# Kernel optimization log

Hardware: AMD Instinct MI355X
Metric: run time of the kernel (lower is better)

## Reference

```python
import jax, jax.numpy as jnp
import numpy as np

FEAT_STRIDE = 16
ANCHOR_SCALES = (8.0, 16.0, 32.0)
ANCHOR_RATIOS = (0.5, 1.0, 2.0)
PRE_NMS_TOPN = 12000
POST_NMS_TOPN = 2000
NMS_THRESH = 0.7
MIN_SIZE = 16.0


def _mkanchors(ws, hs, cx, cy):
    return np.stack([cx - 0.5 * (ws - 1), cy - 0.5 * (hs - 1),
                     cx + 0.5 * (ws - 1), cy + 0.5 * (hs - 1)], axis=1)


def generate_anchors(base_size=16, ratios=ANCHOR_RATIOS, scales=ANCHOR_SCALES):
    ratios = np.asarray(ratios, np.float32)
    scales = np.asarray(scales, np.float32)
    w = h = float(base_size)
    cx = cy = 0.5 * (base_size - 1)
    size = w * h
    ws = np.round(np.sqrt(size / ratios))
    hs = np.round(ws * ratios)
    ratio_anchors = _mkanchors(ws, hs, cx, cy)
    out = []
    for a in ratio_anchors:
        aw = a[2] - a[0] + 1.0
        ah = a[3] - a[1] + 1.0
        acx = a[0] + 0.5 * (aw - 1)
        acy = a[1] + 0.5 * (ah - 1)
        out.append(_mkanchors(aw * scales, ah * scales, acx, acy))
    return np.concatenate(out, axis=0).astype(np.float32)  # (A, 4)


ANCHORS = generate_anchors(FEAT_STRIDE)
NUM_ANCHORS = ANCHORS.shape[0]  # 9


def _proposal_forward(scores, bbox_deltas, im_info):
    A = NUM_ANCHORS
    fg = scores[:, A:, :, :]                       # (1, A, H, W) foreground scores
    H, W = fg.shape[-2], fg.shape[-1]
    im_h, im_w, im_scale = im_info[0, 0], im_info[0, 1], im_info[0, 2]

    # anchor grid
    sx = jnp.arange(W, dtype=jnp.float32) * FEAT_STRIDE
    sy = jnp.arange(H, dtype=jnp.float32) * FEAT_STRIDE
    gy, gx = jnp.meshgrid(sy, sx, indexing='ij')
    shifts = jnp.stack([gx.ravel(), gy.ravel(), gx.ravel(), gy.ravel()], axis=1)  # (K,4)
    anchors = jnp.asarray(ANCHORS)[None, :, :] + shifts[:, None, :]
    anchors = anchors.reshape(-1, 4)               # (K*A, 4)

    deltas = jnp.transpose(bbox_deltas, (0, 2, 3, 1)).reshape(-1, 4)
    sc = jnp.transpose(fg, (0, 2, 3, 1)).reshape(-1)

    # bbox_transform_inv
    aw = anchors[:, 2] - anchors[:, 0] + 1.0
    ah = anchors[:, 3] - anchors[:, 1] + 1.0
    acx = anchors[:, 0] + 0.5 * aw
    acy = anchors[:, 1] + 0.5 * ah
    pcx = deltas[:, 0] * aw + acx
    pcy = deltas[:, 1] * ah + acy
    pw = jnp.exp(deltas[:, 2]) * aw
    ph = jnp.exp(deltas[:, 3]) * ah
    x1 = pcx - 0.5 * pw
    y1 = pcy - 0.5 * ph
    x2 = pcx + 0.5 * pw
    y2 = pcy + 0.5 * ph

    # clip_boxes (scale slot in the clip call is 1.0 in the original)
    x1 = jnp.clip(x1, 0.0, im_w - 1.0)
    x2 = jnp.clip(x2, 0.0, im_w - 1.0)
    y1 = jnp.clip(y1, 0.0, im_h - 1.0)
    y2 = jnp.clip(y2, 0.0, im_h - 1.0)
    props = jnp.stack([x1, y1, x2, y2], axis=1)

    # _filter_boxes: mask instead of gather (jit-safe fixed shapes)
    ms = MIN_SIZE * im_scale
    valid = ((x2 - x1 + 1.0) >= ms) & ((y2 - y1 + 1.0) >= ms)
    sc_m = jnp.where(valid, sc, -jnp.inf)

    # descending sort + pre-NMS top-k in one shot
    top_sc, order = jax.lax.top_k(sc_m, PRE_NMS_TOPN)
    p = props[order]                               # (preN, 4) sorted by score desc
    vk = valid[order]

    pn = jax.lax.stop_gradient(p)
    areas = (pn[:, 2] - pn[:, 0] + 1.0) * (pn[:, 3] - pn[:, 1] + 1.0)
    xx1 = jnp.maximum(pn[:, 0][:, None], pn[:, 0][None, :])
    yy1 = jnp.maximum(pn[:, 1][:, None], pn[:, 1][None, :])
    xx2 = jnp.minimum(pn[:, 2][:, None], pn[:, 2][None, :])
    yy2 = jnp.minimum(pn[:, 3][:, None], pn[:, 3][None, :])
    inter = jnp.maximum(xx2 - xx1 + 1.0, 0.0) * jnp.maximum(yy2 - yy1 + 1.0, 0.0)
    iou = inter / (areas[:, None] + areas[None, :] - inter)
    sup_mat = iou > NMS_THRESH                     # (preN, preN) bool

    idx = jnp.arange(PRE_NMS_TOPN, dtype=jnp.int32)

    def body(keep, xs):
        sup_row, i = xs
        keep = jnp.where(keep[i], keep & ~(sup_row & (idx > i)), keep)
        return keep, None

    keep, _ = jax.lax.scan(body, vk, (sup_mat, idx))

    # keep[:post_nms_topN] with fixed shapes: rank kept boxes, scatter into slots
    rank = jnp.cumsum(keep.astype(jnp.int32)) - 1
    slot_src = jnp.where(keep & (rank < POST_NMS_TOPN), rank, POST_NMS_TOPN)
    slots = jnp.full((POST_NMS_TOPN,), PRE_NMS_TOPN, jnp.int32).at[slot_src].set(idx, mode='drop')

    p_pad = jnp.concatenate([p, jnp.zeros((1, 4), p.dtype)], axis=0)
    s_pad = jnp.concatenate([top_sc, jnp.zeros((1,), top_sc.dtype)], axis=0)
    boxes = p_pad[slots]
    out_sc = s_pad[slots][:, None]
    rois = jnp.concatenate([jnp.zeros((POST_NMS_TOPN, 1), boxes.dtype), boxes], axis=1)
    return rois, out_sc


def setup_inputs() -> dict:
    key = jax.random.key(0)
    k1, k2 = jax.random.split(key)
    H = W = 512
    scores = jax.random.normal(k1, (1, 2 * NUM_ANCHORS, H, W), jnp.float32)
    bbox_deltas = jax.random.normal(k2, (1, 4 * NUM_ANCHORS, H, W), jnp.float32) * 0.2
    im_info = jnp.array([[float(H * FEAT_STRIDE), float(W * FEAT_STRIDE), 1.0]], jnp.float32)
    return {"scores": scores, "bbox_deltas": bbox_deltas, "im_info": im_info}


def reference(scores, bbox_deltas, im_info):
    return _proposal_forward(scores, bbox_deltas, im_info)
```

## Files before the change

kernel.cpp:

```cpp
#include <hip/hip_runtime.h>
#include <hip/hip_bf16.h>
#include <stdint.h>

#pragma clang fp contract(off)

#define FH 512
#define FW 512
#define NA 9
#define HW (FH*FW)
#define TOTAL (HW*NA)
#define PRE_NMS 12000
#define POST_NMS 2000
#define NMS_WORDS 188
#define MT 12032
#define CAND_MAX 16384
#define NMS_TH 0.7f
#define MIN_SIZE_C 16.0f

__constant__ float ANCH[NA][4] = {
  {-84.f,-40.f,99.f,55.f},
  {-176.f,-88.f,191.f,103.f},
  {-360.f,-184.f,375.f,199.f},
  {-56.f,-56.f,71.f,71.f},
  {-120.f,-120.f,135.f,135.f},
  {-248.f,-248.f,263.f,263.f},
  {-36.f,-80.f,51.f,95.f},
  {-80.f,-168.f,95.f,183.f},
  {-168.f,-344.f,183.f,359.f}
};

__device__ __forceinline__ void decode_box(int a, int h, int w,
    const float* __restrict__ deltas, float im_h, float im_w,
    float& x1, float& y1, float& x2, float& y2) {
  float sx = (float)(w * 16);
  float sy = (float)(h * 16);
  float ax1 = ANCH[a][0] + sx;
  float ay1 = ANCH[a][1] + sy;
  float ax2 = ANCH[a][2] + sx;
  float ay2 = ANCH[a][3] + sy;
  float aw = ax2 - ax1 + 1.0f;
  float ah = ay2 - ay1 + 1.0f;
  float acx = ax1 + 0.5f * aw;
  float acy = ay1 + 0.5f * ah;
  int base = h * FW + w;
  float d0 = deltas[(4*a+0)*HW + base];
  float d1 = deltas[(4*a+1)*HW + base];
  float d2 = deltas[(4*a+2)*HW + base];
  float d3 = deltas[(4*a+3)*HW + base];
  float pcx = d0 * aw + acx;
  float pcy = d1 * ah + acy;
  float pw = expf(d2) * aw;
  float ph = expf(d3) * ah;
  x1 = pcx - 0.5f * pw;
  y1 = pcy - 0.5f * ph;
  x2 = pcx + 0.5f * pw;
  y2 = pcy + 0.5f * ph;
  x1 = fminf(fmaxf(x1, 0.0f), im_w - 1.0f);
  x2 = fminf(fmaxf(x2, 0.0f), im_w - 1.0f);
  y1 = fminf(fmaxf(y1, 0.0f), im_h - 1.0f);
  y2 = fminf(fmaxf(y2, 0.0f), im_h - 1.0f);
}

__global__ void k_keys(const float* __restrict__ scores, const float* __restrict__ deltas,
                       const float* __restrict__ im_info, unsigned* __restrict__ keys,
                       unsigned* __restrict__ hist8) {
  __shared__ unsigned lh[256];
  int t = threadIdx.x;
  lh[t] = 0;
  __syncthreads();
  int base = blockIdx.x * blockDim.x + t;
  float im_h = im_info[0], im_w = im_info[1];
  float ms = MIN_SIZE_C * im_info[2];
  int h = base / FW, w = base % FW;
  for (int a = 0; a < NA; a++) {
    float x1, y1, x2, y2;
    decode_box(a, h, w, deltas, im_h, im_w, x1, y1, x2, y2);
    bool valid = ((x2 - x1 + 1.0f) >= ms) && ((y2 - y1 + 1.0f) >= ms);
    float sc = scores[(NA + a)*HW + base];
    float v = valid ? sc : -INFINITY;
    unsigned u = __float_as_uint(v);
    unsigned mono = (u & 0x80000000u) ? ~u : (u | 0x80000000u);
    keys[base*NA + a] = mono;
    atomicAdd(&lh[mono >> 24], 1u);
  }
  __syncthreads();
  atomicAdd(&hist8[t], lh[t]);
}

__global__ void __launch_bounds__(256) k_refine15(const unsigned* __restrict__ keys,
    const unsigned* __restrict__ hist8, unsigned* __restrict__ hist15) {
  __shared__ unsigned ssum[256];
  __shared__ unsigned sB8;
  int t = threadIdx.x;
  unsigned hv = hist8[t];
  ssum[t] = hv;
  __syncthreads();
  for (int off = 1; off < 256; off <<= 1) {
    unsigned v = ssum[t];
    unsigned add = (t + off < 256) ? ssum[t + off] : 0u;
    __syncthreads();
    ssum[t] = v + add;
    __syncthreads();
  }
  unsigned above = ssum[t] - hv;
  if (above < PRE_NMS && above + hv >= PRE_NMS) sB8 = (unsigned)t;
  __syncthreads();
  unsigned B8 = sB8;
  int stride = gridDim.x * blockDim.x;
  for (int i = blockIdx.x * blockDim.x + t; i < TOTAL; i += stride) {
    unsigned k = keys[i];
    if ((k >> 24) == B8) atomicAdd(&hist15[(k >> 9) & 0x7FFFu], 1u);
  }
}

__global__ void __launch_bounds__(256) k_compact(const unsigned* __restrict__ keys,
    const unsigned* __restrict__ hist8, const unsigned* __restrict__ hist15,
    unsigned* __restrict__ cnt, unsigned long long* __restrict__ cand) {
  __shared__ unsigned ssum[256];
  __shared__ unsigned sB8, sT2, sB15;
  int t = threadIdx.x;
  unsigned hv = hist8[t];
  ssum[t] = hv;
  __syncthreads();
  for (int off = 1; off < 256; off <<= 1) {
    unsigned v = ssum[t];
    unsigned add = (t + off < 256) ? ssum[t + off] : 0u;
    __syncthreads();
    ssum[t] = v + add;
    __syncthreads();
  }
  unsigned above = ssum[t] - hv;
  if (above < PRE_NMS && above + hv >= PRE_NMS) { sB8 = (unsigned)t; sT2 = PRE_NMS - above; }
  __syncthreads();
  unsigned B8 = sB8, T2 = sT2;
  unsigned loc = 0;
  for (int i = 0; i < 128; i++) loc += hist15[t*128 + i];
  __syncthreads();
  ssum[t] = loc;
  __syncthreads();
  for (int off = 1; off < 256; off <<= 1) {
    unsigned v = ssum[t];
    unsigned add = (t + off < 256) ? ssum[t + off] : 0u;
    __syncthreads();
    ssum[t] = v + add;
    __syncthreads();
  }
  unsigned above15 = ssum[t] - loc;
  unsigned acc = above15;
  for (int i = 127; i >= 0; i--) {
    unsigned cb = hist15[t*128 + i];
    acc += cb;
    if (acc >= T2 && acc - cb < T2) sB15 = (unsigned)(t*128 + i);
  }
  __syncthreads();
  unsigned K = (B8 << 24) | (sB15 << 9);
  int stride = gridDim.x * blockDim.x;
  for (int i = blockIdx.x * blockDim.x + t; i < TOTAL; i += stride) {
    unsigned k = keys[i];
    if (k >= K) {
      unsigned pos = atomicAdd(cnt, 1u);
      if (pos < CAND_MAX)
        cand[pos] = ((unsigned long long)k << 32) | (unsigned)(~(unsigned)i);
    }
  }
}

__global__ void __launch_bounds__(256) k_rank(const unsigned* __restrict__ pcnt,
    const unsigned long long* __restrict__ cand,
    const float* __restrict__ deltas, const float* __restrict__ im_info,
    float4* __restrict__ boxes, float* __restrict__ scoresArr,
    unsigned long long* __restrict__ remvInit) {
  __shared__ unsigned long long tile[2048];
  unsigned cnt = *pcnt;
  if (cnt > CAND_MAX) cnt = CAND_MAX;
  int i = blockIdx.x * 256 + threadIdx.x;
  unsigned long long mine = (i < (int)cnt) ? cand[i] : 0ULL;
  int rank = 0;
  for (unsigned t0 = 0; t0 < cnt; t0 += 2048) {
    unsigned n = min(2048u, cnt - t0);
    __syncthreads();
    for (unsigned j = threadIdx.x; j < n; j += 256) tile[j] = cand[t0 + j];
    __syncthreads();
    if (i < (int)cnt) {
      unsigned j = 0;
      #pragma unroll 8
      for (; j < n; j++) rank += (tile[j] > mine) ? 1 : 0;
    }
  }
  if (i < (int)cnt && rank < PRE_NMS) {
    unsigned mono = (unsigned)(mine >> 32);
    unsigned idx = ~(unsigned)(mine & 0xFFFFFFFFull);
    unsigned u = (mono & 0x80000000u) ? (mono ^ 0x80000000u) : ~mono;
    float sc = __uint_as_float(u);
    int a = idx % NA;
    int base = idx / NA;
    int h = base / FW, w = base % FW;
    float x1, y1, x2, y2;
    decode_box(a, h, w, deltas, im_info[0], im_info[1], x1, y1, x2, y2);
    boxes[rank] = make_float4(x1, y1, x2, y2);
    scoresArr[rank] = sc;
    if (!(sc > -INFINITY)) atomicOr(&remvInit[rank >> 6], 1ULL << (rank & 63));
  }
}

__global__ void k_mask(const float4* __restrict__ boxes, unsigned long long* __restrict__ maskT) {
  int bi = blockIdx.y, bj = blockIdx.x;
  if (bj < bi) return;
  __shared__ float4 jb[64];
  int t = threadIdx.x;
  int jg = bj * 64 + t;
  jb[t] = (jg < PRE_NMS) ? boxes[jg] : make_float4(0.f, 0.f, -1.f, -1.f);
  __syncthreads();
  int i = bi * 64 + t;
  if (i >= PRE_NMS) return;
  float4 b = boxes[i];
  float area_i = (b.z - b.x + 1.0f) * (b.w - b.y + 1.0f);
  unsigned long long bits = 0;
  for (int jj = 0; jj < 64; jj++) {
    float4 o = jb[jj];
    float xx1 = fmaxf(b.x, o.x);
    float yy1 = fmaxf(b.y, o.y);
    float xx2 = fminf(b.z, o.z);
    float yy2 = fminf(b.w, o.w);
    float iw = fmaxf(xx2 - xx1 + 1.0f, 0.0f);
    float ih = fmaxf(yy2 - yy1 + 1.0f, 0.0f);
    float inter = iw * ih;
    float area_o = (o.z - o.x + 1.0f) * (o.w - o.y + 1.0f);
    float iou = inter / (area_i + area_o - inter);
    if (iou > NMS_TH) bits |= (1ULL << jj);
  }
  maskT[(size_t)bj * MT + i] = bits;
}

__global__ void __launch_bounds__(64) k_nms(const unsigned long long* __restrict__ maskT,
    const unsigned long long* __restrict__ remvInit,
    const float4* __restrict__ boxes, const float* __restrict__ scoresArr,
    float* __restrict__ out) {
  int lane = threadIdx.x;
  __shared__ unsigned klist[POST_NMS];
  __shared__ unsigned long long gbuf[32 * 128];
  int kept_cnt = 0;
  bool done = false;
  unsigned long long W = remvInit[0];
  unsigned long long diagc = maskT[lane];
  unsigned long long nwc   = maskT[(size_t)MT + lane];
  for (int c = 0; c < NMS_WORDS; c++) {
    bool more = (c + 1 < NMS_WORDS);
    int kc = kept_cnt;
    int nIss = more ? ((kc + 63) >> 6) : 0;
    for (int ii = 0; ii < nIss; ii++) {
      int q = ii * 64 + lane;
      if (q < kc) {
        unsigned j = klist[q];
        const void* g = (const void*)(maskT + (size_t)(c + 1) * MT + (j & ~1u));
        void* l = (void*)((char*)gbuf + ii * 1024);
        __builtin_amdgcn_global_load_lds(
            (const __attribute__((address_space(1))) unsigned*)g,
            (__attribute__((address_space(3))) unsigned*)l, 16, 0, 0);
      }
    }
    unsigned long long diagN = 0, nwN = 0;
    if (more) {
      diagN = maskT[(size_t)(c + 1) * MT + (c + 1) * 64 + lane];
      if (c + 2 < NMS_WORDS) nwN = maskT[(size_t)(c + 2) * MT + (c + 1) * 64 + lane];
    }
    int gi0 = c * 64;
    int jmax = PRE_NMS - gi0; if (jmax > 64) jmax = 64;
    unsigned long long avail = ~W;
    if (jmax < 64) avail &= ((1ULL << jmax) - 1ULL);
    unsigned long long keptmask = 0;
    while (avail) {
      int j = __ffsll((long long)avail) - 1;
      keptmask |= (1ULL << j);
      if (lane == 0) klist[kept_cnt] = (unsigned)(gi0 + j);
      kept_cnt++;
      if (kept_cnt >= POST_NMS) { done = true; break; }
      unsigned long long supp = __shfl(diagc, j);
      avail &= ~supp;
      avail &= ~((2ULL << j) - 1ULL);
    }
    if (done || !more) break;
    unsigned long long x = ((keptmask >> lane) & 1ULL) ? nwc : 0ULL;
    asm volatile("s_waitcnt vmcnt(0)" ::: "memory");
    for (int ii = 0; ii < nIss; ii++) {
      int q = ii * 64 + lane;
      if (q < kc) {
        unsigned j = klist[q];
        x |= gbuf[ii * 128 + lane * 2 + (j & 1u)];
      }
    }
    for (int off = 32; off; off >>= 1) x |= __shfl_xor(x, off);
    W = x | remvInit[c + 1];
    __syncthreads();
    diagc = diagN; nwc = nwN;
  }
  __syncthreads();
  for (int s = lane; s < POST_NMS; s += 64) {
    float x1 = 0.f, y1 = 0.f, x2 = 0.f, y2 = 0.f, sc = 0.f;
    if (s < kept_cnt) {
      unsigned r = klist[s];
      float4 b = boxes[r];
      x1 = b.x; y1 = b.y; x2 = b.z; y2 = b.w;
      sc = scoresArr[r];
    }
    out[s*5 + 0] = 0.f;
    out[s*5 + 1] = x1;
    out[s*5 + 2] = y1;
    out[s*5 + 3] = x2;
    out[s*5 + 4] = y2;
    out[POST_NMS*5 + s] = sc;
  }
}

extern "C" void kernel_launch(void* const* d_in, const int* in_sizes, int n_in,
                              void* d_out, int out_size, void* d_ws, size_t ws_size,
                              hipStream_t stream) {
  const float* scores  = (const float*)d_in[0];
  const float* deltas  = (const float*)d_in[1];
  const float* im_info = (const float*)d_in[2];
  float* out = (float*)d_out;
  char* ws = (char*)d_ws;

  unsigned* keys             = (unsigned*)(ws + 0);
  unsigned* hist8            = (unsigned*)(ws + 9437184);
  unsigned* hist15           = (unsigned*)(ws + 9438208);
  unsigned* scal             = (unsigned*)(ws + 9569280);
  unsigned long long* remvI  = (unsigned long long*)(ws + 9569536);
  unsigned long long* cand   = (unsigned long long*)(ws + 9571072);
  float4* boxes              = (float4*)(ws + 9702144);
  float* scoresArr           = (float*)(ws + 9894144);
  unsigned long long* maskT  = (unsigned long long*)(ws + 9942144);

  hipMemsetAsync(ws + 9437184, 0, 133888, stream);

  k_keys<<<HW/256, 256, 0, stream>>>(scores, deltas, im_info, keys, hist8);
  k_refine15<<<256, 256, 0, stream>>>(keys, hist8, hist15);
  k_compact<<<256, 256, 0, stream>>>(keys, hist8, hist15, &scal[4], cand);
  k_rank<<<CAND_MAX/256, 256, 0, stream>>>(&scal[4], cand, deltas, im_info,
                                           boxes, scoresArr, remvI);
  dim3 mg(NMS_WORDS, NMS_WORDS);
  k_mask<<<mg, 64, 0, stream>>>(boxes, maskT);
  k_nms<<<1, 64, 0, stream>>>(maskT, remvI, boxes, scoresArr, out);
}
```

Measured before the change: 907.2 us.

## Switch NMS mask to row-major layout and accumulate suppression rows in registers

The IoU mask is now stored row-major, with 192 words per box, instead of column-transposed, and k_mask computes 8 column words per workgroup. The single-workgroup NMS loop now stages each newly kept box's full mask row into LDS with global_load_lds. It ORs those rows into per-lane register accumulators, replacing the old per-column gather over every kept box. The remove-init bitmap is now memset to ones and cleared for valid boxes with atomicAnd, and the rank count loop uses four accumulators. The aim is to cut the serial NMS loop's per-iteration work from a cost that grows with the kept count to one row load per newly kept box. The trade-off is more LDS traffic and dynamic shared memory.

```diff
diff --git a/kernel.cpp b/kernel.cpp
--- a/kernel.cpp
+++ b/kernel.cpp
@@ -12,7 +12,7 @@
 #define PRE_NMS 12000
 #define POST_NMS 2000
 #define NMS_WORDS 188
-#define MT 12032
+#define MROW 192
 #define CAND_MAX 16384
 #define NMS_TH 0.7f
 #define MIN_SIZE_C 16.0f
@@ -182,9 +182,17 @@
     for (unsigned j = threadIdx.x; j < n; j += 256) tile[j] = cand[t0 + j];
     __syncthreads();
     if (i < (int)cnt) {
+      int q0 = 0, q1 = 0, q2 = 0, q3 = 0;
       unsigned j = 0;
-      #pragma unroll 8
-      for (; j < n; j++) rank += (tile[j] > mine) ? 1 : 0;
+      #pragma unroll 4
+      for (; j + 4 <= n; j += 4) {
+        q0 += (tile[j]   > mine) ? 1 : 0;
+        q1 += (tile[j+1] > mine) ? 1 : 0;
+        q2 += (tile[j+2] > mine) ? 1 : 0;
+        q3 += (tile[j+3] > mine) ? 1 : 0;
+      }
+      for (; j < n; j++) q0 += (tile[j] > mine) ? 1 : 0;
+      rank += q0 + q1 + q2 + q3;
     }
   }
   if (i < (int)cnt && rank < PRE_NMS) {
@@ -199,70 +207,75 @@
     decode_box(a, h, w, deltas, im_info[0], im_info[1], x1, y1, x2, y2);
     boxes[rank] = make_float4(x1, y1, x2, y2);
     scoresArr[rank] = sc;
-    if (!(sc > -INFINITY)) atomicOr(&remvInit[rank >> 6], 1ULL << (rank & 63));
-  }
-}
-
-__global__ void k_mask(const float4* __restrict__ boxes, unsigned long long* __restrict__ maskT) {
-  int bi = blockIdx.y, bj = blockIdx.x;
-  if (bj < bi) return;
-  __shared__ float4 jb[64];
+    if (sc > -INFINITY)
+      atomicAnd(&remvInit[rank >> 6], ~(1ULL << (rank & 63)));
+  }
+}
+
+__global__ void __launch_bounds__(64) k_mask(const float4* __restrict__ boxes,
+                                             unsigned long long* __restrict__ mask) {
+  int wg = blockIdx.x;
+  int bi = blockIdx.y;
+  if (wg * 8 + 7 < bi) return;
+  __shared__ float4 jb[8][64];
   int t = threadIdx.x;
-  int jg = bj * 64 + t;
-  jb[t] = (jg < PRE_NMS) ? boxes[jg] : make_float4(0.f, 0.f, -1.f, -1.f);
+  #pragma unroll
+  for (int k = 0; k < 8; k++) {
+    int jg = (wg * 8 + k) * 64 + t;
+    jb[k][t] = (jg < PRE_NMS) ? boxes[jg] : make_float4(0.f, 0.f, -1.f, -1.f);
+  }
   __syncthreads();
   int i = bi * 64 + t;
   if (i >= PRE_NMS) return;
   float4 b = boxes[i];
   float area_i = (b.z - b.x + 1.0f) * (b.w - b.y + 1.0f);
-  unsigned long long bits = 0;
-  for (int jj = 0; jj < 64; jj++) {
-    float4 o = jb[jj];
-    float xx1 = fmaxf(b.x, o.x);
-    float yy1 = fmaxf(b.y, o.y);
-    float xx2 = fminf(b.z, o.z);
-    float yy2 = fminf(b.w, o.w);
-    float iw = fmaxf(xx2 - xx1 + 1.0f, 0.0f);
-    float ih = fmaxf(yy2 - yy1 + 1.0f, 0.0f);
-    float inter = iw * ih;
-    float area_o = (o.z - o.x + 1.0f) * (o.w - o.y + 1.0f);
-    float iou = inter / (area_i + area_o - inter);
-    if (iou > NMS_TH) bits |= (1ULL << jj);
-  }
-  maskT[(size_t)bj * MT + i] = bits;
-}
-
-__global__ void __launch_bounds__(64) k_nms(const unsigned long long* __restrict__ maskT,
-    const unsigned long long* __restrict__ remvInit,
+  unsigned long long bits[8];
+  #pragma unroll
+  for (int k = 0; k < 8; k++) {
+    unsigned long long bb = 0;
+    for (int jj = 0; jj < 64; jj++) {
+      float4 o = jb[k][jj];
+      float xx1 = fmaxf(b.x, o.x);
+      float yy1 = fmaxf(b.y, o.y);
+      float xx2 = fminf(b.z, o.z);
+      float yy2 = fminf(b.w, o.w);
+      float iw = fmaxf(xx2 - xx1 + 1.0f, 0.0f);
+      float ih = fmaxf(yy2 - yy1 + 1.0f, 0.0f);
+      float inter = iw * ih;
+      float area_o = (o.z - o.x + 1.0f) * (o.w - o.y + 1.0f);
+      float iou = inter / (area_i + area_o - inter);
+      if (iou > NMS_TH) bb |= (1ULL << jj);
+    }
+    bits[k] = bb;
+  }
+  size_t rb = (size_t)i * MROW + wg * 8;
+  #pragma unroll
+  for (int k = 0; k < 8; k++) mask[rb + k] = bits[k];
+}
+
+__global__ void __launch_bounds__(64) k_nms(const unsigned long long* __restrict__ mask,
+    const unsigned long long* __restrict__ remvI,
     const float4* __restrict__ boxes, const float* __restrict__ scoresArr,
     float* __restrict__ out) {
+  extern __shared__ unsigned long long dyn[];
+  unsigned long long* stage = dyn;
+  unsigned* klist = (unsigned*)(dyn + 64 * MROW);
   int lane = threadIdx.x;
-  __shared__ unsigned klist[POST_NMS];
-  __shared__ unsigned long long gbuf[32 * 128];
-  int kept_cnt = 0;
+  unsigned long long r0 = remvI[lane];
+  unsigned long long r1 = remvI[64 + lane];
+  unsigned long long r2 = remvI[128 + lane];
+  unsigned long long W = __shfl(r0, 0);
+  unsigned long long diagc = mask[(size_t)lane * MROW + 0];
+  unsigned long long nw1c  = mask[(size_t)lane * MROW + 1];
+  int kept_cnt = 0, nkPrev = 0;
   bool done = false;
-  unsigned long long W = remvInit[0];
-  unsigned long long diagc = maskT[lane];
-  unsigned long long nwc   = maskT[(size_t)MT + lane];
   for (int c = 0; c < NMS_WORDS; c++) {
     bool more = (c + 1 < NMS_WORDS);
-    int kc = kept_cnt;
-    int nIss = more ? ((kc + 63) >> 6) : 0;
-    for (int ii = 0; ii < nIss; ii++) {
-      int q = ii * 64 + lane;
-      if (q < kc) {
-        unsigned j = klist[q];
-        const void* g = (const void*)(maskT + (size_t)(c + 1) * MT + (j & ~1u));
-        void* l = (void*)((char*)gbuf + ii * 1024);
-        __builtin_amdgcn_global_load_lds(
-            (const __attribute__((address_space(1))) unsigned*)g,
-            (__attribute__((address_space(3))) unsigned*)l, 16, 0, 0);
-      }
-    }
-    unsigned long long diagN = 0, nwN = 0;
+    unsigned long long diagN = 0, nw1N = 0;
     if (more) {
-      diagN = maskT[(size_t)(c + 1) * MT + (c + 1) * 64 + lane];
-      if (c + 2 < NMS_WORDS) nwN = maskT[(size_t)(c + 2) * MT + (c + 1) * 64 + lane];
+      size_t rb = (size_t)((c + 1) * 64 + lane) * MROW;
+      diagN = mask[rb + (c + 1)];
+      if (c + 2 < NMS_WORDS) nw1N = mask[rb + (c + 2)];
     }
     int gi0 = c * 64;
     int jmax = PRE_NMS - gi0; if (jmax > 64) jmax = 64;
@@ -280,19 +293,37 @@
       avail &= ~((2ULL << j) - 1ULL);
     }
     if (done || !more) break;
-    unsigned long long x = ((keptmask >> lane) & 1ULL) ? nwc : 0ULL;
+    unsigned long long A = ((keptmask >> lane) & 1ULL) ? nw1c : 0ULL;
     asm volatile("s_waitcnt vmcnt(0)" ::: "memory");
-    for (int ii = 0; ii < nIss; ii++) {
-      int q = ii * 64 + lane;
-      if (q < kc) {
-        unsigned j = klist[q];
-        x |= gbuf[ii * 128 + lane * 2 + (j & 1u)];
-      }
-    }
+    __builtin_amdgcn_sched_barrier(0);
+    for (int s = 0; s < nkPrev; s++) {
+      r0 |= stage[s * MROW + lane];
+      r1 |= stage[s * MROW + 64 + lane];
+      r2 |= stage[s * MROW + 128 + lane];
+    }
+    unsigned long long x = A;
+    #pragma unroll
     for (int off = 32; off; off >>= 1) x |= __shfl_xor(x, off);
-    W = x | remvInit[c + 1];
-    __syncthreads();
-    diagc = diagN; nwc = nwN;
+    int cw = c + 1;
+    unsigned long long Rw = ((cw >> 6) == 0) ? r0 : (((cw >> 6) == 1) ? r1 : r2);
+    W = __shfl(Rw, cw & 63) | x;
+    int slot = 0;
+    unsigned long long km = keptmask;
+    while (km) {
+      int j = __ffsll((long long)km) - 1; km &= km - 1;
+      const char* rb = (const char*)(mask + (size_t)(gi0 + j) * MROW);
+      char* lb = (char*)(void*)stage + slot * 1536;
+      __builtin_amdgcn_global_load_lds(
+          (const __attribute__((address_space(1))) unsigned*)(rb + lane * 16),
+          (__attribute__((address_space(3))) unsigned*)lb, 16, 0, 0);
+      if (lane < 30)
+        __builtin_amdgcn_global_load_lds(
+            (const __attribute__((address_space(1))) unsigned*)(rb + 1024 + lane * 16),
+            (__attribute__((address_space(3))) unsigned*)(lb + 1024), 16, 0, 0);
+      slot++;
+    }
+    nkPrev = slot;
+    diagc = diagN; nw1c = nw1N;
   }
   __syncthreads();
   for (int s = lane; s < POST_NMS; s += 64) {
@@ -329,16 +360,20 @@
   unsigned long long* cand   = (unsigned long long*)(ws + 9571072);
   float4* boxes              = (float4*)(ws + 9702144);
   float* scoresArr           = (float*)(ws + 9894144);
-  unsigned long long* maskT  = (unsigned long long*)(ws + 9942144);
-
-  hipMemsetAsync(ws + 9437184, 0, 133888, stream);
+  unsigned long long* mask   = (unsigned long long*)(ws + 9942144);
+
+  hipMemsetAsync(ws + 9437184, 0, 132352, stream);
+  hipMemsetAsync(ws + 9569536, 0xFF, 1536, stream);
 
   k_keys<<<HW/256, 256, 0, stream>>>(scores, deltas, im_info, keys, hist8);
   k_refine15<<<256, 256, 0, stream>>>(keys, hist8, hist15);
   k_compact<<<256, 256, 0, stream>>>(keys, hist8, hist15, &scal[4], cand);
   k_rank<<<CAND_MAX/256, 256, 0, stream>>>(&scal[4], cand, deltas, im_info,
                                            boxes, scoresArr, remvI);
-  dim3 mg(NMS_WORDS, NMS_WORDS);
-  k_mask<<<mg, 64, 0, stream>>>(boxes, maskT);
-  k_nms<<<1, 64, 0, stream>>>(maskT, remvI, boxes, scoresArr, out);
-}
+  dim3 mg(24, 188);
+  k_mask<<<mg, 64, 0, stream>>>(boxes, mask);
+
+  (void)hipFuncSetAttribute((const void*)k_nms,
+        hipFuncAttributeMaxDynamicSharedMemorySize, 64*MROW*8 + 2000*4);
+  k_nms<<<1, 64, 64*MROW*8 + 2000*4, stream>>>(mask, remvI, boxes, scoresArr, out);
+}
```

Result: slower. 1.012 ms (+11.5%).
